# Performance work log

Hardware: AMD Instinct MI355X
Metric: run time of the kernel (lower is better)

Reference implementation:

```python
import jax, jax.numpy as jnp
import numpy as np

MAX_LEN = 128
VOCAB = 32000
SENTINEL = 2**30  # larger than any valid token id; pushes masked slots to the end after sort


def setup_inputs() -> dict:
    key = jax.random.key(0)
    k1, k2, k3, k4 = jax.random.split(key, 4)
    B, L = 262144, MAX_LEN
    input_ids = jax.random.randint(k1, (B, L), 0, VOCAB, dtype=jnp.int32)
    attention_mask = jax.random.randint(k2, (B, L), 0, 2, dtype=jnp.int32)
    # MLP params: Linear(3,32) -> ReLU -> Linear(32,32) -> ReLU
    W1 = jax.random.normal(k3, (3, 32), dtype=jnp.float32) * (1.0 / np.sqrt(3.0))
    b1 = jnp.zeros((32,), dtype=jnp.float32)
    W2 = jax.random.normal(k4, (32, 32), dtype=jnp.float32) * (1.0 / np.sqrt(32.0))
    b2 = jnp.zeros((32,), dtype=jnp.float32)
    return {"input_ids": input_ids, "attention_mask": attention_mask,
            "W1": W1, "b1": b1, "W2": W2, "b2": b2}


def _symbolic_feats(input_ids, attention_mask):
    # Batched replacement of the per-row torch.unique loop:
    # sort masked tokens per row, count boundaries between distinct values.
    mask = attention_mask.astype(bool)
    seq_len = jnp.sum(mask, axis=1)  # [B]
    ids_m = jnp.where(mask, input_ids, SENTINEL)  # masked-out slots -> sentinel
    s = jnp.sort(ids_m, axis=1)  # valid tokens first (ids < SENTINEL)
    valid = s < SENTINEL
    first = jnp.ones((s.shape[0], 1), dtype=bool)
    new_val = jnp.concatenate([first, s[:, 1:] != s[:, :-1]], axis=1)
    uniq = jnp.sum(valid & new_val, axis=1)  # [B] unique count among valid tokens
    seq_f = seq_len.astype(jnp.float32)
    uniq_f = uniq.astype(jnp.float32)
    uniq_ratio = jnp.where(seq_len > 0, uniq_f / jnp.maximum(seq_f, 1.0), 0.0)
    feats = jnp.stack([seq_f / MAX_LEN, uniq_f / MAX_LEN, uniq_ratio], axis=1)  # [B,3]
    return feats


def reference(input_ids, attention_mask, W1, b1, W2, b2):
    feats = _symbolic_feats(input_ids, attention_mask)  # [B,3]
    h = jax.nn.relu(feats @ W1 + b1)
    out = jax.nn.relu(h @ W2 + b2)
    return out
```

## Files before the change

### kernel.cpp

```cpp
#include <hip/hip_runtime.h>

#define ROW_LEN 128
#define NPAIR (129 * 129)

__global__ __launch_bounds__(256) void mlp_table_kernel(
    const float* __restrict__ W1, const float* __restrict__ b1,
    const float* __restrict__ W2, const float* __restrict__ b2,
    float* __restrict__ table)
{
    const int tid = blockIdx.x * 256 + threadIdx.x;
    if (tid >= NPAIR * 32) return;
    const int p = tid >> 5;
    const int j = tid & 31;
    const int seq  = p / 129;
    const int uniq = p % 129;
    const float f0 = (float)seq  * (1.0f / 128.0f);
    const float f1 = (float)uniq * (1.0f / 128.0f);
    const float f2 = (seq > 0) ? ((float)uniq / (float)seq) : 0.0f;

    float acc = b2[j];
    #pragma unroll
    for (int jj = 0; jj < 32; ++jj) {
        float h = b1[jj];
        h = fmaf(f0, W1[jj],      h);
        h = fmaf(f1, W1[32 + jj], h);
        h = fmaf(f2, W1[64 + jj], h);
        h = fmaxf(h, 0.0f);
        acc = fmaf(h, W2[jj * 32 + j], acc);
    }
    table[tid] = fmaxf(acc, 0.0f);
}

__global__ __launch_bounds__(256, 8) void rows_kernel(
    const int* __restrict__ ids, const int* __restrict__ amask,
    const float* __restrict__ table, float* __restrict__ out, int B)
{
    __shared__ unsigned bm[4][1024];

    const int wave = threadIdx.x >> 6;
    const int lane = threadIdx.x & 63;
    unsigned* mybm = bm[wave];

    {
        uint4* z = (uint4*)mybm;
        #pragma unroll
        for (int i = 0; i < 4; ++i) z[lane + i * 64] = make_uint4(0u, 0u, 0u, 0u);
    }

    const long W  = (long)gridDim.x * 4;
    long row = (long)blockIdx.x * 4 + wave;
    if (row >= B) return;

    int2 id2 = ((const int2*)ids)[row * 64 + lane];
    int2 mk2 = ((const int2*)amask)[row * 64 + lane];

    for (; row < B; row += W) {
        const long nrow = (row + W < (long)B) ? (row + W) : row;
        const int2 nid = ((const int2*)ids)[nrow * 64 + lane];
        const int2 nmk = ((const int2*)amask)[nrow * 64 + lane];

        int n0 = 0, n1 = 0;
        if (mk2.x != 0) {
            const unsigned t = (unsigned)id2.x, m = 1u << (t & 31u);
            n0 = ((atomicOr(&mybm[t >> 5], m) & m) == 0u);
        }
        if (mk2.y != 0) {
            const unsigned t = (unsigned)id2.y, m = 1u << (t & 31u);
            n1 = ((atomicOr(&mybm[t >> 5], m) & m) == 0u);
        }

        if (mk2.x != 0) mybm[(unsigned)id2.x >> 5] = 0u;
        if (mk2.y != 0) mybm[(unsigned)id2.y >> 5] = 0u;

        const unsigned long long s0 = __ballot(mk2.x != 0);
        const unsigned long long s1 = __ballot(mk2.y != 0);
        const unsigned long long u0 = __ballot(n0 != 0);
        const unsigned long long u1 = __ballot(n1 != 0);

        const int seq  = __popcll(s0) + __popcll(s1);
        const int uniq = __popcll(u0) + __popcll(u1);

        const int p = seq * 129 + uniq;
        if (lane < 32) {
            __builtin_nontemporal_store(table[p * 32 + lane],
                                        &out[row * 32 + lane]);
        }

        id2 = nid; mk2 = nmk;
    }
}

extern "C" void kernel_launch(void* const* d_in, const int* in_sizes, int n_in,
                              void* d_out, int out_size, void* d_ws, size_t ws_size,
                              hipStream_t stream) {
    const int*   ids   = (const int*)d_in[0];
    const int*   amask = (const int*)d_in[1];
    const float* W1    = (const float*)d_in[2];
    const float* b1    = (const float*)d_in[3];
    const float* W2    = (const float*)d_in[4];
    const float* b2    = (const float*)d_in[5];
    float* out   = (float*)d_out;
    float* table = (float*)d_ws;

    const int B = in_sizes[0] / ROW_LEN;

    const int tblThreads = NPAIR * 32;
    mlp_table_kernel<<<(tblThreads + 255) / 256, 256, 0, stream>>>(W1, b1, W2, b2, table);

    int blocks = (B + 3) / 4;
    if (blocks > 2048) blocks = 2048;
    rows_kernel<<<blocks, 256, 0, stream>>>(ids, amask, table, out, B);
}
```

Measured before the change: 294.0 us.

## Software-pipeline row processing in batches of four with double-buffered loads

Restructures the rows kernel so each wave handles four rows per batch, double-buffering the global loads of ids and mask, and overlapping the table gather and output store of one batch with processing of the next. The bitmap is now fully zeroed with vector stores before each row instead of clearing only the touched words afterward. Nontemporal stores are replaced by ordinary stores. This exposes more memory-level parallelism for a bandwidth-bound kernel, at the cost of more registers and extra LDS zeroing work per row.

New measurement: 458.2 us. 55.9% more time.

```diff
diff --git a/kernel.cpp b/kernel.cpp
--- a/kernel.cpp
+++ b/kernel.cpp
@@ -31,34 +31,43 @@
     table[tid] = fmaxf(acc, 0.0f);
 }
 
-__global__ __launch_bounds__(256, 8) void rows_kernel(
-    const int* __restrict__ ids, const int* __restrict__ amask,
-    const float* __restrict__ table, float* __restrict__ out, int B)
+struct Batch {
+    int2 id[4];
+    int2 mk[4];
+};
+
+__device__ __forceinline__ void load_batch(
+    const int2* ids2, const int2* mk2v, long r0, long stride, long k, long B,
+    int lane, Batch& b)
 {
-    __shared__ unsigned bm[4][1024];
+    #pragma unroll
+    for (int j = 0; j < 4; ++j) {
+        const long row = r0 + (k * 4 + j) * stride;
+        if (row < B) {
+            b.id[j] = ids2[row * 64 + lane];
+            b.mk[j] = mk2v[row * 64 + lane];
+        } else {
+            b.id[j] = make_int2(0, 0);
+            b.mk[j] = make_int2(0, 0);
+        }
+    }
+}
 
-    const int wave = threadIdx.x >> 6;
-    const int lane = threadIdx.x & 63;
-    unsigned* mybm = bm[wave];
+__device__ __forceinline__ void proc_batch(
+    unsigned* mybm, int lane, long r0, long stride, long k, long B,
+    const Batch& b, int* p)
+{
+    #pragma unroll
+    for (int j = 0; j < 4; ++j) {
+        const long row = r0 + (k * 4 + j) * stride;
+        if (row >= B) { p[j] = 0; continue; }
 
-    {
         uint4* z = (uint4*)mybm;
         #pragma unroll
         for (int i = 0; i < 4; ++i) z[lane + i * 64] = make_uint4(0u, 0u, 0u, 0u);
-    }
 
-    const long W  = (long)gridDim.x * 4;
-    long row = (long)blockIdx.x * 4 + wave;
-    if (row >= B) return;
-
-    int2 id2 = ((const int2*)ids)[row * 64 + lane];
-    int2 mk2 = ((const int2*)amask)[row * 64 + lane];
-
-    for (; row < B; row += W) {
-        const long nrow = (row + W < (long)B) ? (row + W) : row;
-        const int2 nid = ((const int2*)ids)[nrow * 64 + lane];
-        const int2 nmk = ((const int2*)amask)[nrow * 64 + lane];
-
+        const int2 id2 = b.id[j];
+        const int2 mk2 = b.mk[j];
         int n0 = 0, n1 = 0;
         if (mk2.x != 0) {
             const unsigned t = (unsigned)id2.x, m = 1u << (t & 31u);
@@ -69,9 +78,6 @@
             n1 = ((atomicOr(&mybm[t >> 5], m) & m) == 0u);
         }
 
-        if (mk2.x != 0) mybm[(unsigned)id2.x >> 5] = 0u;
-        if (mk2.y != 0) mybm[(unsigned)id2.y >> 5] = 0u;
-
         const unsigned long long s0 = __ballot(mk2.x != 0);
         const unsigned long long s1 = __ballot(mk2.y != 0);
         const unsigned long long u0 = __ballot(n0 != 0);
@@ -79,15 +85,81 @@
 
         const int seq  = __popcll(s0) + __popcll(s1);
         const int uniq = __popcll(u0) + __popcll(u1);
+        p[j] = seq * 129 + uniq;
+    }
+}
 
-        const int p = seq * 129 + uniq;
-        if (lane < 32) {
-            __builtin_nontemporal_store(table[p * 32 + lane],
-                                        &out[row * 32 + lane]);
+__device__ __forceinline__ void gather_batch(const float* __restrict__ table,
+                                             int lane, const int* p, float* g)
+{
+    if (lane < 32) {
+        #pragma unroll
+        for (int j = 0; j < 4; ++j) g[j] = table[p[j] * 32 + lane];
+    }
+}
+
+__device__ __forceinline__ void store_batch(float* __restrict__ out, int lane,
+    long r0, long stride, long k, long B, const float* g)
+{
+    if (lane < 32) {
+        #pragma unroll
+        for (int j = 0; j < 4; ++j) {
+            const long row = r0 + (k * 4 + j) * stride;
+            if (row < B) out[row * 32 + lane] = g[j];
         }
+    }
+}
 
-        id2 = nid; mk2 = nmk;
+__global__ __launch_bounds__(256, 8) void rows_kernel(
+    const int* __restrict__ ids, const int* __restrict__ amask,
+    const float* __restrict__ table, float* __restrict__ out, int B)
+{
+    __shared__ unsigned bm[4][1024];
+    const int wave = threadIdx.x >> 6;
+    const int lane = threadIdx.x & 63;
+    unsigned* mybm = bm[wave];
+    const int2* ids2 = (const int2*)ids;
+    const int2* mk2v = (const int2*)amask;
+
+    const long stride = (long)gridDim.x * 4;
+    const long r0 = (long)blockIdx.x * 4 + wave;
+    const long nb = (((long)B + stride - 1) / stride + 3) / 4;
+    if (nb <= 0 || r0 >= B) return;
+
+    Batch bA, bBv;
+    int p[4], pn[4];
+    float g[4];
+
+    load_batch(ids2, mk2v, r0, stride, 0, B, lane, bA);
+    load_batch(ids2, mk2v, r0, stride, 1, B, lane, bBv);
+    proc_batch(mybm, lane, r0, stride, 0, B, bA, p);
+
+    long k = 1;
+    for (; k + 1 < nb; k += 2) {
+        gather_batch(table, lane, p, g);
+        load_batch(ids2, mk2v, r0, stride, k + 1, B, lane, bA);
+        proc_batch(mybm, lane, r0, stride, k, B, bBv, pn);
+        store_batch(out, lane, r0, stride, k - 1, B, g);
+        #pragma unroll
+        for (int j = 0; j < 4; ++j) p[j] = pn[j];
+
+        gather_batch(table, lane, p, g);
+        load_batch(ids2, mk2v, r0, stride, k + 2, B, lane, bBv);
+        proc_batch(mybm, lane, r0, stride, k + 1, B, bA, pn);
+        store_batch(out, lane, r0, stride, k, B, g);
+        #pragma unroll
+        for (int j = 0; j < 4; ++j) p[j] = pn[j];
     }
+    if (k < nb) {
+        gather_batch(table, lane, p, g);
+        proc_batch(mybm, lane, r0, stride, k, B, bBv, pn);
+        store_batch(out, lane, r0, stride, k - 1, B, g);
+        #pragma unroll
+        for (int j = 0; j < 4; ++j) p[j] = pn[j];
+        ++k;
+    }
+    gather_batch(table, lane, p, g);
+    store_batch(out, lane, r0, stride, k - 1, B, g);
 }
 
 extern "C" void kernel_launch(void* const* d_in, const int* in_sizes, int n_in,
```

## Software-pipeline row loop two rows at a time with deeper prefetch

Applied to the files above, without the earlier changes.

Restructures the per-wave row loop to handle two rows per step, with the next four rows' ids and masks prefetched into registers. The table gather for the previous pair overlaps with the bitmap processing of the current pair, and a tail loop covers leftover rows. Bitmap clearing now zeroes the whole 4KB per-wave bitmap before every row instead of clearing only the touched words, which adds LDS write traffic. Output stores switch from nontemporal to plain stores. The aim is to hide global-load latency in what looks like a latency-bound streaming loop, at the cost of more registers and more LDS work.

New measurement: 299.9 us. 1.02x slower.

```diff
diff --git a/kernel.cpp b/kernel.cpp
--- a/kernel.cpp
+++ b/kernel.cpp
@@ -31,62 +31,111 @@
     table[tid] = fmaxf(acc, 0.0f);
 }
 
+__device__ __forceinline__ int proc_row(unsigned* mybm, int lane, int2 id2, int2 mk2)
+{
+    uint4* z = (uint4*)mybm;
+    #pragma unroll
+    for (int i = 0; i < 4; ++i) z[lane + i * 64] = make_uint4(0u, 0u, 0u, 0u);
+
+    int n0 = 0, n1 = 0;
+    if (mk2.x != 0) {
+        const unsigned t = (unsigned)id2.x, m = 1u << (t & 31u);
+        n0 = ((atomicOr(&mybm[t >> 5], m) & m) == 0u);
+    }
+    if (mk2.y != 0) {
+        const unsigned t = (unsigned)id2.y, m = 1u << (t & 31u);
+        n1 = ((atomicOr(&mybm[t >> 5], m) & m) == 0u);
+    }
+    const unsigned long long s0 = __ballot(mk2.x != 0);
+    const unsigned long long s1 = __ballot(mk2.y != 0);
+    const unsigned long long u0 = __ballot(n0 != 0);
+    const unsigned long long u1 = __ballot(n1 != 0);
+    const int seq  = __popcll(s0) + __popcll(s1);
+    const int uniq = __popcll(u0) + __popcll(u1);
+    return seq * 129 + uniq;
+}
+
 __global__ __launch_bounds__(256, 8) void rows_kernel(
     const int* __restrict__ ids, const int* __restrict__ amask,
     const float* __restrict__ table, float* __restrict__ out, int B)
 {
     __shared__ unsigned bm[4][1024];
-
     const int wave = threadIdx.x >> 6;
     const int lane = threadIdx.x & 63;
     unsigned* mybm = bm[wave];
+    const int2* ids2 = (const int2*)ids;
+    const int2* mk2v = (const int2*)amask;
 
-    {
-        uint4* z = (uint4*)mybm;
-        #pragma unroll
-        for (int i = 0; i < 4; ++i) z[lane + i * 64] = make_uint4(0u, 0u, 0u, 0u);
+    const unsigned nw = gridDim.x * 4;
+    const unsigned w  = blockIdx.x * 4 + wave;
+    const unsigned S  = nw * 64;
+    const unsigned OS = nw * 32;
+    const unsigned nb = ((unsigned)B % (2u * nw) == 0u) ? (unsigned)B / (2u * nw) : 0u;
+
+    unsigned li = w * 64 + lane;
+    unsigned oi = w * 32 + lane;
+
+    int2 xi0, xm0, xi1, xm1;
+    int2 yi0, ym0, yi1, ym1;
+    int p0 = 0, p1 = 0;
+    float g0 = 0.0f, g1 = 0.0f;
+
+    if (nb > 0) {
+        xi0 = ids2[li];          xm0 = mk2v[li];
+        xi1 = ids2[li + S];      xm1 = mk2v[li + S];
+        if (nb > 1) {
+            yi0 = ids2[li + 2 * S]; ym0 = mk2v[li + 2 * S];
+            yi1 = ids2[li + 3 * S]; ym1 = mk2v[li + 3 * S];
+        }
+        unsigned pf = li + 4 * S;
+
+        p0 = proc_row(mybm, lane, xi0, xm0);
+        p1 = proc_row(mybm, lane, xi1, xm1);
+
+        unsigned k = 1;
+        for (; k + 1 < nb; k += 2) {
+            if (lane < 32) { g0 = table[p0 * 32 + lane]; g1 = table[p1 * 32 + lane]; }
+            xi0 = ids2[pf];     xm0 = mk2v[pf];
+            xi1 = ids2[pf + S]; xm1 = mk2v[pf + S];
+            pf += 2 * S;
+            int q0 = proc_row(mybm, lane, yi0, ym0);
+            int q1 = proc_row(mybm, lane, yi1, ym1);
+            if (lane < 32) { out[oi] = g0; out[oi + OS] = g1; }
+            oi += 2 * OS;
+            p0 = q0; p1 = q1;
+
+            if (lane < 32) { g0 = table[p0 * 32 + lane]; g1 = table[p1 * 32 + lane]; }
+            if (k + 2 < nb) {
+                yi0 = ids2[pf];     ym0 = mk2v[pf];
+                yi1 = ids2[pf + S]; ym1 = mk2v[pf + S];
+                pf += 2 * S;
+            }
+            q0 = proc_row(mybm, lane, xi0, xm0);
+            q1 = proc_row(mybm, lane, xi1, xm1);
+            if (lane < 32) { out[oi] = g0; out[oi + OS] = g1; }
+            oi += 2 * OS;
+            p0 = q0; p1 = q1;
+        }
+        if (k < nb) {
+            if (lane < 32) { g0 = table[p0 * 32 + lane]; g1 = table[p1 * 32 + lane]; }
+            int q0 = proc_row(mybm, lane, yi0, ym0);
+            int q1 = proc_row(mybm, lane, yi1, ym1);
+            if (lane < 32) { out[oi] = g0; out[oi + OS] = g1; }
+            oi += 2 * OS;
+            p0 = q0; p1 = q1;
+        }
+        if (lane < 32) {
+            out[oi]      = table[p0 * 32 + lane];
+            out[oi + OS] = table[p1 * 32 + lane];
+        }
     }
 
-    const long W  = (long)gridDim.x * 4;
-    long row = (long)blockIdx.x * 4 + wave;
-    if (row >= B) return;
-
-    int2 id2 = ((const int2*)ids)[row * 64 + lane];
-    int2 mk2 = ((const int2*)amask)[row * 64 + lane];
-
-    for (; row < B; row += W) {
-        const long nrow = (row + W < (long)B) ? (row + W) : row;
-        const int2 nid = ((const int2*)ids)[nrow * 64 + lane];
-        const int2 nmk = ((const int2*)amask)[nrow * 64 + lane];
-
-        int n0 = 0, n1 = 0;
-        if (mk2.x != 0) {
-            const unsigned t = (unsigned)id2.x, m = 1u << (t & 31u);
-            n0 = ((atomicOr(&mybm[t >> 5], m) & m) == 0u);
-        }
-        if (mk2.y != 0) {
-            const unsigned t = (unsigned)id2.y, m = 1u << (t & 31u);
-            n1 = ((atomicOr(&mybm[t >> 5], m) & m) == 0u);
-        }
-
-        if (mk2.x != 0) mybm[(unsigned)id2.x >> 5] = 0u;
-        if (mk2.y != 0) mybm[(unsigned)id2.y >> 5] = 0u;
-
-        const unsigned long long s0 = __ballot(mk2.x != 0);
-        const unsigned long long s1 = __ballot(mk2.y != 0);
-        const unsigned long long u0 = __ballot(n0 != 0);
-        const unsigned long long u1 = __ballot(n1 != 0);
-
-        const int seq  = __popcll(s0) + __popcll(s1);
-        const int uniq = __popcll(u0) + __popcll(u1);
-
-        const int p = seq * 129 + uniq;
-        if (lane < 32) {
-            __builtin_nontemporal_store(table[p * 32 + lane],
-                                        &out[row * 32 + lane]);
-        }
-
-        id2 = nid; mk2 = nmk;
+    for (unsigned row = w + nb * 2 * nw; row < (unsigned)B; row += nw) {
+        const unsigned idx = row * 64 + lane;
+        const int2 id2 = ids2[idx];
+        const int2 mk2 = mk2v[idx];
+        const int p = proc_row(mybm, lane, id2, mk2);
+        if (lane < 32) out[row * 32 + lane] = table[p * 32 + lane];
     }
 }
 
```
